# Performance work log

Measured on AMD Instinct MI355X. Metric: run time of the kernel, lower is better.

Reference implementation:

```python
import jax, jax.numpy as jnp
import numpy as np

N_NODES = 50000
N_EDGES = 800000
D_IN = 64
D_OUT = 64


def setup_inputs() -> dict:
    key = jax.random.key(0)
    ks = jax.random.split(key, 5)
    feat = jax.random.normal(ks[0], (N_NODES, D_IN), dtype=jnp.float32)
    src = jax.random.randint(ks[1], (N_EDGES,), 0, N_NODES, dtype=jnp.int64)
    dst = jax.random.randint(ks[2], (N_EDGES,), 0, N_NODES, dtype=jnp.int64)
    # Xavier-uniform-ish scale for weights
    lim = float(np.sqrt(6.0 / (D_IN + D_OUT)) * np.sqrt(2.0))
    W_neigh = jax.random.uniform(ks[3], (D_OUT, D_IN), dtype=jnp.float32, minval=-lim, maxval=lim)
    W_self = jax.random.uniform(ks[4], (D_OUT, D_IN), dtype=jnp.float32, minval=-lim, maxval=lim)
    b_self = jnp.zeros((D_OUT,), dtype=jnp.float32)
    return {"feat": feat, "src": src, "dst": dst,
            "W_neigh": W_neigh, "W_self": W_self, "b_self": b_self}


def reference(feat, src, dst, W_neigh, W_self, b_self):
    # srcdata = fc_neigh(feat_src)  -> [N, D_OUT]
    srcdata = feat @ W_neigh.T
    # A_div.T @ srcdata == mean of transformed source feats over in-edges per dst.
    # deg[j] = A.sum(0)[j]; column scaling by 1/deg then transpose-SpMM.
    agg = jax.ops.segment_sum(srcdata[src], dst, num_segments=N_NODES)  # [N, D_OUT]
    deg = jax.ops.segment_sum(jnp.ones_like(dst, dtype=srcdata.dtype), dst,
                              num_segments=N_NODES)  # [N]
    # Zero-degree columns stay zero in the sparse product (no stored nonzeros).
    dstdata = jnp.where(deg[:, None] > 0, agg / jnp.maximum(deg, 1.0)[:, None], 0.0)
    # rst = fc_self(feat_dst) + dstdata ; feat_dst = feat[:N_dst] = feat (square A)
    return feat @ W_self.T + b_self + dstdata
```

## Files before the change

### kernel.cpp

```cpp
#include <hip/hip_runtime.h>

#define N_NODES 50000
#define N_EDGES 800000
#define D 64
#define RB 64
#define NBUCK 782
#define CHUNK 2048
#define NCHUNK 391
#define SUBCAP 24
#define NFEATBLK 3125
#define SCAP 1536
#define ALD 68
#define ZID N_NODES
#define FQW (N_NODES * D / 4 + D / 4)

typedef __attribute__((ext_vector_type(8))) __bf16 bf16x8;
typedef __attribute__((ext_vector_type(4))) float f32x4;
typedef __attribute__((ext_vector_type(2))) float f32x2;

__device__ inline unsigned f2bf(float f) {
    unsigned b = __builtin_bit_cast(unsigned, f);
    b += 0x7fffu + ((b >> 16) & 1u);
    return b >> 16;
}

__device__ inline void acc16p(f32x2* a, uint4 v) {
    a[0] += __builtin_amdgcn_cvt_pk_f32_fp8((int)v.x, false);
    a[1] += __builtin_amdgcn_cvt_pk_f32_fp8((int)v.x, true);
    a[2] += __builtin_amdgcn_cvt_pk_f32_fp8((int)v.y, false);
    a[3] += __builtin_amdgcn_cvt_pk_f32_fp8((int)v.y, true);
    a[4] += __builtin_amdgcn_cvt_pk_f32_fp8((int)v.z, false);
    a[5] += __builtin_amdgcn_cvt_pk_f32_fp8((int)v.z, true);
    a[6] += __builtin_amdgcn_cvt_pk_f32_fp8((int)v.w, false);
    a[7] += __builtin_amdgcn_cvt_pk_f32_fp8((int)v.w, true);
}

__global__ __launch_bounds__(256) void prep_scatter_kernel(
        const float* __restrict__ feat, const float* __restrict__ Wn, const float* __restrict__ Ws,
        const int* __restrict__ src, const int* __restrict__ dst,
        unsigned* __restrict__ fq,
        unsigned short* __restrict__ wnb, unsigned short* __restrict__ wsb,
        unsigned int* __restrict__ ebuf, unsigned char* __restrict__ cntArr) {
    __shared__ int cntB[NBUCK];
    int b = blockIdx.x;
    int t = threadIdx.x;
    if (b < NCHUNK) {
        for (int i = t; i < NBUCK; i += 256) cntB[i] = 0;
        __syncthreads();
        int e0 = b * CHUNK;
#pragma unroll
        for (int k = 0; k < 8; ++k) {
            int e = e0 + k * 256 + t;
            if (e < N_EDGES) {
                int dv = dst[e];
                int bk = dv >> 6;
                int slot = atomicAdd(&cntB[bk], 1);
                if (slot < SUBCAP)
                    ebuf[((size_t)bk * NCHUNK + b) * SUBCAP + slot] =
                        (unsigned)src[e] | ((unsigned)(dv & (RB - 1)) << 16);
            }
        }
        __syncthreads();
        for (int i = t; i < NBUCK; i += 256) {
            int c = cntB[i];
            cntArr[(size_t)b * NBUCK + i] = (unsigned char)(c < SUBCAP ? c : SUBCAP);
        }
    } else if (b < NCHUNK + NFEATBLK) {
        int i = (b - NCHUNK) * 256 + t;
        float4 v = ((const float4*)feat)[i];
        int q = __builtin_amdgcn_cvt_pk_fp8_f32(v.x, v.y, 0, false);
        q = __builtin_amdgcn_cvt_pk_fp8_f32(v.z, v.w, q, true);
        fq[i] = (unsigned)q;
    } else {
        for (int i = t; i < D * D; i += 256) {
            wnb[i] = (unsigned short)f2bf(Wn[i]);
            wsb[i] = (unsigned short)f2bf(Ws[i]);
        }
        if (t < D / 4) fq[(size_t)N_NODES * (D / 4) + t] = 0u;
    }
}

__global__ __launch_bounds__(256) void gather_mfma_kernel(
        const float* __restrict__ feat, const unsigned char* __restrict__ fq,
        const unsigned int* __restrict__ ebuf, const unsigned char* __restrict__ cntArr,
        const unsigned short* __restrict__ wsb, const unsigned short* __restrict__ wnb,
        const float* __restrict__ bias, float* __restrict__ out) {
    __shared__ int cnt[RB];
    __shared__ int cur[RB];
    __shared__ int base[RB];
    __shared__ unsigned short sorted[SCAP];
    __shared__ float agg[RB * ALD];
    int t = threadIdx.x;
    int bk = blockIdx.x;
    if (t < RB) cnt[t] = 0;
    __syncthreads();
    for (int c = t; c < NCHUNK; c += 256) {
        int cc = cntArr[(size_t)c * NBUCK + bk];
        const unsigned int* slab = ebuf + ((size_t)bk * NCHUNK + c) * SUBCAP;
        for (int j = 0; j < cc; j += 4) {
            uint4 v = *(const uint4*)(slab + j);
            atomicAdd(&cnt[(v.x >> 16) & (RB - 1)], 1);
            if (j + 1 < cc) atomicAdd(&cnt[(v.y >> 16) & (RB - 1)], 1);
            if (j + 2 < cc) atomicAdd(&cnt[(v.z >> 16) & (RB - 1)], 1);
            if (j + 3 < cc) atomicAdd(&cnt[(v.w >> 16) & (RB - 1)], 1);
        }
    }
    __syncthreads();
    if (t < RB) {
        int c = cnt[t];
        int pcv = (c + 3) & ~3;
        int s = pcv;
#pragma unroll
        for (int d = 1; d < RB; d <<= 1) {
            int v = __shfl_up(s, d, 64);
            if (t >= d) s += v;
        }
        base[t] = s - pcv;
        cur[t] = s - pcv;
    }
    __syncthreads();
    for (int c = t; c < NCHUNK; c += 256) {
        int cc = cntArr[(size_t)c * NBUCK + bk];
        const unsigned int* slab = ebuf + ((size_t)bk * NCHUNK + c) * SUBCAP;
        for (int j = 0; j < cc; j += 4) {
            uint4 v = *(const uint4*)(slab + j);
            int p;
            p = atomicAdd(&cur[(v.x >> 16) & (RB - 1)], 1);
            if (p < SCAP) sorted[p] = (unsigned short)(v.x & 0xFFFFu);
            if (j + 1 < cc) { p = atomicAdd(&cur[(v.y >> 16) & (RB - 1)], 1); if (p < SCAP) sorted[p] = (unsigned short)(v.y & 0xFFFFu); }
            if (j + 2 < cc) { p = atomicAdd(&cur[(v.z >> 16) & (RB - 1)], 1); if (p < SCAP) sorted[p] = (unsigned short)(v.z & 0xFFFFu); }
            if (j + 3 < cc) { p = atomicAdd(&cur[(v.w >> 16) & (RB - 1)], 1); if (p < SCAP) sorted[p] = (unsigned short)(v.w & 0xFFFFu); }
        }
    }
    if (t < RB) {
        int c = cnt[t];
        int b0 = base[t];
        int pcv = (c + 3) & ~3;
        for (int j = c; j < pcv; ++j)
            if (b0 + j < SCAP) sorted[b0 + j] = (unsigned short)ZID;
    }
    __syncthreads();
    int ns = t >> 2, p = t & 3;
    int dg = cnt[ns];
    int b0 = base[ns];
    int pcn = (dg + 3) & ~3;
    if (b0 + pcn > SCAP) pcn = (b0 < SCAP) ? ((SCAP - b0) & ~3) : 0;
    f32x2 acc2[8];
#pragma unroll
    for (int j = 0; j < 8; ++j) acc2[j] = (f32x2){0.f, 0.f};
    const unsigned char* fqp = fq + p * 16;
    for (int i = 0; i < pcn; i += 4) {
        int id0 = sorted[b0 + i + 0];
        int id1 = sorted[b0 + i + 1];
        int id2 = sorted[b0 + i + 2];
        int id3 = sorted[b0 + i + 3];
        uint4 v0 = *(const uint4*)(fqp + (size_t)id0 * D);
        uint4 v1 = *(const uint4*)(fqp + (size_t)id1 * D);
        uint4 v2 = *(const uint4*)(fqp + (size_t)id2 * D);
        uint4 v3 = *(const uint4*)(fqp + (size_t)id3 * D);
        acc16p(acc2, v0); acc16p(acc2, v1); acc16p(acc2, v2); acc16p(acc2, v3);
    }
    float inv = (dg > 0) ? 1.0f / (float)dg : 0.f;
    float* ap = &agg[ns * ALD + p * 16];
#pragma unroll
    for (int j = 0; j < 4; ++j) {
        float4 o = make_float4(acc2[2 * j].x * inv, acc2[2 * j].y * inv,
                               acc2[2 * j + 1].x * inv, acc2[2 * j + 1].y * inv);
        *(float4*)(ap + 4 * j) = o;
    }
    __syncthreads();
    int r0 = blockIdx.x * RB;
    int w = t >> 6, lane = t & 63;
    int m = lane & 15, quad = lane >> 4;
    int row = r0 + 16 * w + m;
    int rowA = row < N_NODES ? row : N_NODES - 1;
    const float* fr = feat + (size_t)rowA * D + quad * 8;
    float4 f0 = *(const float4*)(fr + 0);
    float4 f1 = *(const float4*)(fr + 4);
    float4 f2 = *(const float4*)(fr + 32);
    float4 f3 = *(const float4*)(fr + 36);
    bf16x8 aS0, aS1, aA0, aA1;
    aS0[0] = (__bf16)f0.x; aS0[1] = (__bf16)f0.y; aS0[2] = (__bf16)f0.z; aS0[3] = (__bf16)f0.w;
    aS0[4] = (__bf16)f1.x; aS0[5] = (__bf16)f1.y; aS0[6] = (__bf16)f1.z; aS0[7] = (__bf16)f1.w;
    aS1[0] = (__bf16)f2.x; aS1[1] = (__bf16)f2.y; aS1[2] = (__bf16)f2.z; aS1[3] = (__bf16)f2.w;
    aS1[4] = (__bf16)f3.x; aS1[5] = (__bf16)f3.y; aS1[6] = (__bf16)f3.z; aS1[7] = (__bf16)f3.w;
#pragma unroll
    for (int j = 0; j < 8; ++j) {
        aA0[j] = (__bf16)agg[(16 * w + m) * ALD + 0  + quad * 8 + j];
        aA1[j] = (__bf16)agg[(16 * w + m) * ALD + 32 + quad * 8 + j];
    }
#pragma unroll
    for (int tt = 0; tt < 4; ++tt) {
        int nn = 16 * tt + m;
        bf16x8 bS0 = *(const bf16x8*)(wsb + (size_t)nn * D + 0  + quad * 8);
        bf16x8 bS1 = *(const bf16x8*)(wsb + (size_t)nn * D + 32 + quad * 8);
        bf16x8 bN0 = *(const bf16x8*)(wnb + (size_t)nn * D + 0  + quad * 8);
        bf16x8 bN1 = *(const bf16x8*)(wnb + (size_t)nn * D + 32 + quad * 8);
        f32x4 cc4 = {0.f, 0.f, 0.f, 0.f};
        cc4 = __builtin_amdgcn_mfma_f32_16x16x32_bf16(aS0, bS0, cc4, 0, 0, 0);
        cc4 = __builtin_amdgcn_mfma_f32_16x16x32_bf16(aS1, bS1, cc4, 0, 0, 0);
        cc4 = __builtin_amdgcn_mfma_f32_16x16x32_bf16(aA0, bN0, cc4, 0, 0, 0);
        cc4 = __builtin_amdgcn_mfma_f32_16x16x32_bf16(aA1, bN1, cc4, 0, 0, 0);
        float bv = bias[16 * tt + m];
#pragma unroll
        for (int reg = 0; reg < 4; ++reg) {
            int orow = r0 + 16 * w + quad * 4 + reg;
            if (orow < N_NODES)
                out[(size_t)orow * D + 16 * tt + m] = cc4[reg] + bv;
        }
    }
}

extern "C" void kernel_launch(void* const* d_in, const int* in_sizes, int n_in,
                              void* d_out, int out_size, void* d_ws, size_t ws_size,
                              hipStream_t stream) {
    const float* feat  = (const float*)d_in[0];
    const int*   src   = (const int*)d_in[1];
    const int*   dst   = (const int*)d_in[2];
    const float* Wn    = (const float*)d_in[3];
    const float* Wself = (const float*)d_in[4];
    const float* bself = (const float*)d_in[5];
    float* out = (float*)d_out;

    unsigned*       featq = (unsigned*)d_ws;
    unsigned short* wnb   = (unsigned short*)(featq + FQW);
    unsigned short* wsb   = wnb + D * D;
    unsigned int*   ebuf  = (unsigned int*)(wsb + D * D);
    unsigned char*  cntArr = (unsigned char*)(ebuf + (size_t)NBUCK * NCHUNK * SUBCAP);

    prep_scatter_kernel<<<NCHUNK + NFEATBLK + 1, 256, 0, stream>>>(
        feat, Wn, Wself, src, dst, featq, wnb, wsb, ebuf, cntArr);
    gather_mfma_kernel<<<NBUCK, 256, 0, stream>>>(
        feat, (const unsigned char*)featq, ebuf, cntArr, wsb, wnb, bself, out);
}
```

Baseline: 113.9 us.

## Split each gather bucket across two blocks with eight threads per node

```diff
diff --git a/kernel.cpp b/kernel.cpp
--- a/kernel.cpp
+++ b/kernel.cpp
@@ -11,6 +11,7 @@
 #define NFEATBLK 3125
 #define SCAP 1536
 #define ALD 68
+#define GH 32
 #define ZID N_NODES
 #define FQW (N_NODES * D / 4 + D / 4)
 
@@ -24,15 +25,11 @@
     return b >> 16;
 }
 
-__device__ inline void acc16p(f32x2* a, uint4 v) {
+__device__ inline void acc8p(f32x2* a, uint2 v) {
     a[0] += __builtin_amdgcn_cvt_pk_f32_fp8((int)v.x, false);
     a[1] += __builtin_amdgcn_cvt_pk_f32_fp8((int)v.x, true);
     a[2] += __builtin_amdgcn_cvt_pk_f32_fp8((int)v.y, false);
     a[3] += __builtin_amdgcn_cvt_pk_f32_fp8((int)v.y, true);
-    a[4] += __builtin_amdgcn_cvt_pk_f32_fp8((int)v.z, false);
-    a[5] += __builtin_amdgcn_cvt_pk_f32_fp8((int)v.z, true);
-    a[6] += __builtin_amdgcn_cvt_pk_f32_fp8((int)v.w, false);
-    a[7] += __builtin_amdgcn_cvt_pk_f32_fp8((int)v.w, true);
 }
 
 __global__ __launch_bounds__(256) void prep_scatter_kernel(
@@ -89,9 +86,10 @@
     __shared__ int cur[RB];
     __shared__ int base[RB];
     __shared__ unsigned short sorted[SCAP];
-    __shared__ float agg[RB * ALD];
+    __shared__ float agg[GH * ALD];
     int t = threadIdx.x;
-    int bk = blockIdx.x;
+    int bk = blockIdx.x >> 1;
+    int half = blockIdx.x & 1;
     if (t < RB) cnt[t] = 0;
     __syncthreads();
     for (int c = t; c < NCHUNK; c += 256) {
@@ -140,39 +138,37 @@
             if (b0 + j < SCAP) sorted[b0 + j] = (unsigned short)ZID;
     }
     __syncthreads();
-    int ns = t >> 2, p = t & 3;
-    int dg = cnt[ns];
-    int b0 = base[ns];
+    int ns = t >> 3, p = t & 7;
+    int nl = half * GH + ns;
+    int dg = cnt[nl];
+    int b0 = base[nl];
     int pcn = (dg + 3) & ~3;
     if (b0 + pcn > SCAP) pcn = (b0 < SCAP) ? ((SCAP - b0) & ~3) : 0;
-    f32x2 acc2[8];
-#pragma unroll
-    for (int j = 0; j < 8; ++j) acc2[j] = (f32x2){0.f, 0.f};
-    const unsigned char* fqp = fq + p * 16;
+    f32x2 acc2[4];
+#pragma unroll
+    for (int j = 0; j < 4; ++j) acc2[j] = (f32x2){0.f, 0.f};
+    const unsigned char* fqp = fq + p * 8;
     for (int i = 0; i < pcn; i += 4) {
         int id0 = sorted[b0 + i + 0];
         int id1 = sorted[b0 + i + 1];
         int id2 = sorted[b0 + i + 2];
         int id3 = sorted[b0 + i + 3];
-        uint4 v0 = *(const uint4*)(fqp + (size_t)id0 * D);
-        uint4 v1 = *(const uint4*)(fqp + (size_t)id1 * D);
-        uint4 v2 = *(const uint4*)(fqp + (size_t)id2 * D);
-        uint4 v3 = *(const uint4*)(fqp + (size_t)id3 * D);
-        acc16p(acc2, v0); acc16p(acc2, v1); acc16p(acc2, v2); acc16p(acc2, v3);
+        uint2 v0 = *(const uint2*)(fqp + (size_t)id0 * D);
+        uint2 v1 = *(const uint2*)(fqp + (size_t)id1 * D);
+        uint2 v2 = *(const uint2*)(fqp + (size_t)id2 * D);
+        uint2 v3 = *(const uint2*)(fqp + (size_t)id3 * D);
+        acc8p(acc2, v0); acc8p(acc2, v1); acc8p(acc2, v2); acc8p(acc2, v3);
     }
     float inv = (dg > 0) ? 1.0f / (float)dg : 0.f;
-    float* ap = &agg[ns * ALD + p * 16];
-#pragma unroll
-    for (int j = 0; j < 4; ++j) {
-        float4 o = make_float4(acc2[2 * j].x * inv, acc2[2 * j].y * inv,
-                               acc2[2 * j + 1].x * inv, acc2[2 * j + 1].y * inv);
-        *(float4*)(ap + 4 * j) = o;
-    }
-    __syncthreads();
-    int r0 = blockIdx.x * RB;
+    float* ap = &agg[ns * ALD + p * 8];
+    *(float4*)(ap + 0) = make_float4(acc2[0].x * inv, acc2[0].y * inv, acc2[1].x * inv, acc2[1].y * inv);
+    *(float4*)(ap + 4) = make_float4(acc2[2].x * inv, acc2[2].y * inv, acc2[3].x * inv, acc2[3].y * inv);
+    __syncthreads();
+    int r0 = blockIdx.x * GH;
     int w = t >> 6, lane = t & 63;
     int m = lane & 15, quad = lane >> 4;
-    int row = r0 + 16 * w + m;
+    int tile = w >> 1, th = w & 1;
+    int row = r0 + 16 * tile + m;
     int rowA = row < N_NODES ? row : N_NODES - 1;
     const float* fr = feat + (size_t)rowA * D + quad * 8;
     float4 f0 = *(const float4*)(fr + 0);
@@ -186,11 +182,12 @@
     aS1[4] = (__bf16)f3.x; aS1[5] = (__bf16)f3.y; aS1[6] = (__bf16)f3.z; aS1[7] = (__bf16)f3.w;
 #pragma unroll
     for (int j = 0; j < 8; ++j) {
-        aA0[j] = (__bf16)agg[(16 * w + m) * ALD + 0  + quad * 8 + j];
-        aA1[j] = (__bf16)agg[(16 * w + m) * ALD + 32 + quad * 8 + j];
-    }
-#pragma unroll
-    for (int tt = 0; tt < 4; ++tt) {
+        aA0[j] = (__bf16)agg[(16 * tile + m) * ALD + 0  + quad * 8 + j];
+        aA1[j] = (__bf16)agg[(16 * tile + m) * ALD + 32 + quad * 8 + j];
+    }
+#pragma unroll
+    for (int ti = 0; ti < 2; ++ti) {
+        int tt = th * 2 + ti;
         int nn = 16 * tt + m;
         bf16x8 bS0 = *(const bf16x8*)(wsb + (size_t)nn * D + 0  + quad * 8);
         bf16x8 bS1 = *(const bf16x8*)(wsb + (size_t)nn * D + 32 + quad * 8);
@@ -204,7 +201,7 @@
         float bv = bias[16 * tt + m];
 #pragma unroll
         for (int reg = 0; reg < 4; ++reg) {
-            int orow = r0 + 16 * w + quad * 4 + reg;
+            int orow = r0 + 16 * tile + quad * 4 + reg;
             if (orow < N_NODES)
                 out[(size_t)orow * D + 16 * tt + m] = cc4[reg] + bv;
         }
@@ -230,6 +227,6 @@
 
     prep_scatter_kernel<<<NCHUNK + NFEATBLK + 1, 256, 0, stream>>>(
         feat, Wn, Wself, src, dst, featq, wnb, wsb, ebuf, cntArr);
-    gather_mfma_kernel<<<NBUCK, 256, 0, stream>>>(
+    gather_mfma_kernel<<<2 * NBUCK, 256, 0, stream>>>(
         feat, (const unsigned char*)featq, ebuf, cntArr, wsb, wnb, bself, out);
 }
```

Measured after the change: 121.6 us. 6.7% more time.

## Replace fixed-capacity per-bucket edge slabs with compact per-chunk CSR buckets

Applied to the files above, without the earlier changes.

```diff
diff --git a/kernel.cpp b/kernel.cpp
--- a/kernel.cpp
+++ b/kernel.cpp
@@ -7,7 +7,7 @@
 #define NBUCK 782
 #define CHUNK 2048
 #define NCHUNK 391
-#define SUBCAP 24
+#define OFFP 784
 #define NFEATBLK 3125
 #define SCAP 1536
 #define ALD 68
@@ -40,8 +40,11 @@
         const int* __restrict__ src, const int* __restrict__ dst,
         unsigned* __restrict__ fq,
         unsigned short* __restrict__ wnb, unsigned short* __restrict__ wsb,
-        unsigned int* __restrict__ ebuf, unsigned char* __restrict__ cntArr) {
+        unsigned* __restrict__ epk, unsigned short* __restrict__ offArr) {
     __shared__ int cntB[NBUCK];
+    __shared__ unsigned short offB[NBUCK + 2];
+    __shared__ int wtot[4];
+    __shared__ __align__(16) unsigned rec[CHUNK];
     int b = blockIdx.x;
     int t = threadIdx.x;
     if (b < NCHUNK) {
@@ -51,20 +54,47 @@
 #pragma unroll
         for (int k = 0; k < 8; ++k) {
             int e = e0 + k * 256 + t;
+            if (e < N_EDGES) atomicAdd(&cntB[dst[e] >> 6], 1);
+        }
+        __syncthreads();
+        int i0 = 4 * t;
+        int s0 = (i0 + 0 < NBUCK) ? cntB[i0 + 0] : 0;
+        int s1 = (i0 + 1 < NBUCK) ? cntB[i0 + 1] : 0;
+        int s2 = (i0 + 2 < NBUCK) ? cntB[i0 + 2] : 0;
+        int s3 = (i0 + 3 < NBUCK) ? cntB[i0 + 3] : 0;
+        int ls = s0 + s1 + s2 + s3;
+        int lane = t & 63, w = t >> 6;
+        int ws = ls;
+#pragma unroll
+        for (int d = 1; d < 64; d <<= 1) {
+            int v = __shfl_up(ws, d, 64);
+            if (lane >= d) ws += v;
+        }
+        if (lane == 63) wtot[w] = ws;
+        __syncthreads();
+        int wbase = 0;
+#pragma unroll
+        for (int k = 0; k < 4; ++k) if (k < w) wbase += wtot[k];
+        int r = wbase + ws - ls;
+        if (i0 + 0 < NBUCK) { offB[i0 + 0] = (unsigned short)r; cntB[i0 + 0] = r; r += s0; }
+        if (i0 + 1 < NBUCK) { offB[i0 + 1] = (unsigned short)r; cntB[i0 + 1] = r; r += s1; }
+        if (i0 + 2 < NBUCK) { offB[i0 + 2] = (unsigned short)r; cntB[i0 + 2] = r; r += s2; }
+        if (i0 + 3 < NBUCK) { offB[i0 + 3] = (unsigned short)r; cntB[i0 + 3] = r; r += s3; }
+        if (t == 195) offB[NBUCK] = (unsigned short)r;
+        __syncthreads();
+#pragma unroll
+        for (int k = 0; k < 8; ++k) {
+            int e = e0 + k * 256 + t;
             if (e < N_EDGES) {
                 int dv = dst[e];
-                int bk = dv >> 6;
-                int slot = atomicAdd(&cntB[bk], 1);
-                if (slot < SUBCAP)
-                    ebuf[((size_t)bk * NCHUNK + b) * SUBCAP + slot] =
-                        (unsigned)src[e] | ((unsigned)(dv & (RB - 1)) << 16);
+                int slot = atomicAdd(&cntB[dv >> 6], 1);
+                rec[slot] = (unsigned)src[e] | ((unsigned)(dv & (RB - 1)) << 16);
             }
         }
         __syncthreads();
-        for (int i = t; i < NBUCK; i += 256) {
-            int c = cntB[i];
-            cntArr[(size_t)b * NBUCK + i] = (unsigned char)(c < SUBCAP ? c : SUBCAP);
-        }
+        uint4* dst4 = (uint4*)(epk + (size_t)b * CHUNK);
+        for (int i = t; i < CHUNK / 4; i += 256) dst4[i] = ((const uint4*)rec)[i];
+        for (int i = t; i <= NBUCK; i += 256) offArr[(size_t)b * OFFP + i] = offB[i];
     } else if (b < NCHUNK + NFEATBLK) {
         int i = (b - NCHUNK) * 256 + t;
         float4 v = ((const float4*)feat)[i];
@@ -82,7 +112,7 @@
 
 __global__ __launch_bounds__(256) void gather_mfma_kernel(
         const float* __restrict__ feat, const unsigned char* __restrict__ fq,
-        const unsigned int* __restrict__ ebuf, const unsigned char* __restrict__ cntArr,
+        const unsigned* __restrict__ epk, const unsigned short* __restrict__ offArr,
         const unsigned short* __restrict__ wsb, const unsigned short* __restrict__ wnb,
         const float* __restrict__ bias, float* __restrict__ out) {
     __shared__ int cnt[RB];
@@ -95,15 +125,11 @@
     if (t < RB) cnt[t] = 0;
     __syncthreads();
     for (int c = t; c < NCHUNK; c += 256) {
-        int cc = cntArr[(size_t)c * NBUCK + bk];
-        const unsigned int* slab = ebuf + ((size_t)bk * NCHUNK + c) * SUBCAP;
-        for (int j = 0; j < cc; j += 4) {
-            uint4 v = *(const uint4*)(slab + j);
-            atomicAdd(&cnt[(v.x >> 16) & (RB - 1)], 1);
-            if (j + 1 < cc) atomicAdd(&cnt[(v.y >> 16) & (RB - 1)], 1);
-            if (j + 2 < cc) atomicAdd(&cnt[(v.z >> 16) & (RB - 1)], 1);
-            if (j + 3 < cc) atomicAdd(&cnt[(v.w >> 16) & (RB - 1)], 1);
-        }
+        const unsigned short* offc = offArr + (size_t)c * OFFP;
+        int o0 = offc[bk], o1 = offc[bk + 1];
+        const unsigned* pay = epk + (size_t)c * CHUNK;
+        for (int j = o0; j < o1; ++j)
+            atomicAdd(&cnt[(pay[j] >> 16) & (RB - 1)], 1);
     }
     __syncthreads();
     if (t < RB) {
@@ -120,16 +146,13 @@
     }
     __syncthreads();
     for (int c = t; c < NCHUNK; c += 256) {
-        int cc = cntArr[(size_t)c * NBUCK + bk];
-        const unsigned int* slab = ebuf + ((size_t)bk * NCHUNK + c) * SUBCAP;
-        for (int j = 0; j < cc; j += 4) {
-            uint4 v = *(const uint4*)(slab + j);
-            int p;
-            p = atomicAdd(&cur[(v.x >> 16) & (RB - 1)], 1);
-            if (p < SCAP) sorted[p] = (unsigned short)(v.x & 0xFFFFu);
-            if (j + 1 < cc) { p = atomicAdd(&cur[(v.y >> 16) & (RB - 1)], 1); if (p < SCAP) sorted[p] = (unsigned short)(v.y & 0xFFFFu); }
-            if (j + 2 < cc) { p = atomicAdd(&cur[(v.z >> 16) & (RB - 1)], 1); if (p < SCAP) sorted[p] = (unsigned short)(v.z & 0xFFFFu); }
-            if (j + 3 < cc) { p = atomicAdd(&cur[(v.w >> 16) & (RB - 1)], 1); if (p < SCAP) sorted[p] = (unsigned short)(v.w & 0xFFFFu); }
+        const unsigned short* offc = offArr + (size_t)c * OFFP;
+        int o0 = offc[bk], o1 = offc[bk + 1];
+        const unsigned* pay = epk + (size_t)c * CHUNK;
+        for (int j = o0; j < o1; ++j) {
+            unsigned rr = pay[j];
+            int p = atomicAdd(&cur[(rr >> 16) & (RB - 1)], 1);
+            if (p < SCAP) sorted[p] = (unsigned short)(rr & 0xFFFFu);
         }
     }
     if (t < RB) {
@@ -222,14 +245,14 @@
     const float* bself = (const float*)d_in[5];
     float* out = (float*)d_out;
 
-    unsigned*       featq = (unsigned*)d_ws;
-    unsigned short* wnb   = (unsigned short*)(featq + FQW);
-    unsigned short* wsb   = wnb + D * D;
-    unsigned int*   ebuf  = (unsigned int*)(wsb + D * D);
-    unsigned char*  cntArr = (unsigned char*)(ebuf + (size_t)NBUCK * NCHUNK * SUBCAP);
+    unsigned*       featq  = (unsigned*)d_ws;
+    unsigned short* wnb    = (unsigned short*)(featq + FQW);
+    unsigned short* wsb    = wnb + D * D;
+    unsigned*       epk    = (unsigned*)(wsb + D * D);
+    unsigned short* offArr = (unsigned short*)(epk + (size_t)NCHUNK * CHUNK);
 
     prep_scatter_kernel<<<NCHUNK + NFEATBLK + 1, 256, 0, stream>>>(
-        feat, Wn, Wself, src, dst, featq, wnb, wsb, ebuf, cntArr);
+        feat, Wn, Wself, src, dst, featq, wnb, wsb, epk, offArr);
     gather_mfma_kernel<<<NBUCK, 256, 0, stream>>>(
-        feat, (const unsigned char*)featq, ebuf, cntArr, wsb, wnb, bself, out);
-}
+        feat, (const unsigned char*)featq, epk, offArr, wsb, wnb, bself, out);
+}
```

Result: no change. 115.0 us (+1.0%).
